# Kernel tuning notes

Hardware: AMD Instinct MI355X
Metric: run time of the kernel (lower is better)

Reference implementation:

```python
import jax, jax.numpy as jnp
import numpy as np

SQRT5 = 2.2360679774997896


def setup_inputs() -> dict:
    key = jax.random.key(0)
    k1, k2, k3 = jax.random.split(key, 3)
    n, m, d = 1024, 1024, 8
    X1 = jax.random.normal(k1, (n, d), dtype=jnp.float32)
    X2 = jax.random.normal(k2, (m, d), dtype=jnp.float32)
    c = jnp.asarray(1.0, dtype=jnp.float32)  # overall_scaling (scalar param)
    # character_length: positive lengthscales per feature
    l = 0.5 + jax.random.uniform(k3, (d,), dtype=jnp.float32)
    return {"X1": X1, "X2": X2, "c": c, "l": l}


def reference(X1, X2, c, l):
    # X1: [n, d], X2: [m, d] -> out [n, d, m, d]
    d = l.shape[0]
    inv_l2 = 1.0 / (l * l)                       # [d]
    DX1X2 = X1[:, None, :] - X2[None, :, :]      # [n, m, d]
    # scaled pairwise distance r[i,j] = || (X1_i - X2_j) / l ||
    r = jnp.sqrt(jnp.sum((DX1X2 / l) ** 2, axis=-1))   # [n, m]
    fr = (5.0 / 3.0) * jnp.exp(-SQRT5 * r)             # [n, m]
    # M[a,b] = (1/l^2) * eye(d) with column-wise broadcast (matches torch):
    M = inv_l2 * jnp.eye(d, dtype=l.dtype)             # [d, d], diag = 1/l^2
    A = fr * (1.0 + SQRT5 * r)                         # [n, m]
    D = DX1X2 * inv_l2                                 # [n, m, d]
    # k[i,a,j,b] = A[i,j]*M[a,b] - 5*fr[i,j]*D[i,j,a]*D[i,j,b]
    k = jnp.einsum('ij,ab->iajb', A, M) - 5.0 * jnp.einsum('ij,ija,ijb->iajb', fr, D, D)
    return (c * c) * k
```

## Files before the change

### kernel.cpp

```cpp
#include <hip/hip_runtime.h>

#define SQRT5F 2.2360679774997896f


__global__ __launch_bounds__(256) void deriv2_matern52_kernel(
    const float* __restrict__ X1,
    const float* __restrict__ X2,
    const float* __restrict__ c_ptr,
    const float* __restrict__ l_ptr,
    float* __restrict__ out,
    int m )
{
    const int t = threadIdx.x;
    const int jblocks = m >> 7;
    const int i  = blockIdx.x / jblocks;
    const int jb = blockIdx.x - i * jblocks;
    const int j  = (jb << 7) + (t >> 1);
    const int h  = t & 1;
    const int b0 = h << 2;

    const float c  = c_ptr[0];
    const float c2 = c * c;

    float inv_l2[8];
#pragma unroll
    for (int k = 0; k < 8; ++k) {
        const float lv = l_ptr[k];
        inv_l2[k] = 1.0f / (lv * lv);
    }

    const float4 x1a = ((const float4*)(X1 + (size_t)i * 8))[0];
    const float4 x1b = ((const float4*)(X1 + (size_t)i * 8))[1];
    const float4 x2a = ((const float4*)(X2 + (size_t)j * 8))[0];
    const float4 x2b = ((const float4*)(X2 + (size_t)j * 8))[1];

    const float dx[8] = { x1a.x - x2a.x, x1a.y - x2a.y, x1a.z - x2a.z, x1a.w - x2a.w,
                          x1b.x - x2b.x, x1b.y - x2b.y, x1b.z - x2b.z, x1b.w - x2b.w };

    float D[8];
    float r2 = 0.0f;
#pragma unroll
    for (int k = 0; k < 8; ++k) {
        D[k] = dx[k] * inv_l2[k];
        r2 += dx[k] * D[k];
    }

    const float r  = sqrtf(r2);
    const float fr = (5.0f / 3.0f) * expf(-SQRT5F * r);
    const float A  = fr * (1.0f + SQRT5F * r);

    const float Ac = A * c2;
    const float cf = -5.0f * fr * c2;

    const float Db[4] = { D[b0 + 0], D[b0 + 1], D[b0 + 2], D[b0 + 3] };

    float* op = out + (size_t)i * (size_t)(8 * m * 8) + (size_t)j * 8 + b0;
    const size_t astride = (size_t)m * 8;

#pragma unroll
    for (int a = 0; a < 8; ++a) {
        const float Dca = cf * D[a];
        float v[4];
#pragma unroll
        for (int k = 0; k < 4; ++k) v[k] = Dca * Db[k];
        const int da = a - b0;
        if (da >= 0 && da < 4) v[da] += Ac * inv_l2[a];

        *(float4*)(op + (size_t)a * astride) = make_float4(v[0], v[1], v[2], v[3]);
    }
}

extern "C" void kernel_launch(void* const* d_in, const int* in_sizes, int n_in,
                              void* d_out, int out_size, void* d_ws, size_t ws_size,
                              hipStream_t stream) {
    const float* X1 = (const float*)d_in[0];
    const float* X2 = (const float*)d_in[1];
    const float* c  = (const float*)d_in[2];
    const float* l  = (const float*)d_in[3];
    float* out = (float*)d_out;

    const int d = in_sizes[3];
    const int n = in_sizes[0] / d;
    const int m = in_sizes[1] / d;

    const int jblocks = m >> 7;
    dim3 grid(n * jblocks);
    dim3 block(256);
    deriv2_matern52_kernel<<<grid, block, 0, stream>>>(X1, X2, c, l, out, m);
}
```

Measured before the change: 257.5 us.

## Assign one output row per wavefront and loop over X2 in a persistent block

Each block now handles one X1 row with 512 threads, and each of its 8 wavefronts owns one output 'a' plane. Every lane loops over j in strides of 32 and writes one float4 per iteration, so a wavefront's stores form one contiguous 1KB run instead of eight strided stores per thread. The cost is that the distance and exp math is recomputed 8 times, once per wavefront, and the grid shrinks to n blocks, each running a sequential loop. Branchless selector masks replace the per-thread diagonal branch.

```diff
diff --git a/kernel.cpp b/kernel.cpp
--- a/kernel.cpp
+++ b/kernel.cpp
@@ -3,7 +3,7 @@
 #define SQRT5F 2.2360679774997896f
 
 
-__global__ __launch_bounds__(256) void deriv2_matern52_kernel(
+__global__ __launch_bounds__(512) void deriv2_matern52_kernel(
     const float* __restrict__ X1,
     const float* __restrict__ X2,
     const float* __restrict__ c_ptr,
@@ -11,13 +11,14 @@
     float* __restrict__ out,
     int m )
 {
-    const int t = threadIdx.x;
-    const int jblocks = m >> 7;
-    const int i  = blockIdx.x / jblocks;
-    const int jb = blockIdx.x - i * jblocks;
-    const int j  = (jb << 7) + (t >> 1);
-    const int h  = t & 1;
-    const int b0 = h << 2;
+    const int t    = threadIdx.x;
+    const int w    = t >> 6;
+    const int lane = t & 63;
+    const int p    = lane >> 1;
+    const int h    = lane & 1;
+    const int b0   = h << 2;
+
+    const int i = blockIdx.x;
 
     const float c  = c_ptr[0];
     const float c2 = c * c;
@@ -29,44 +30,67 @@
         inv_l2[k] = 1.0f / (lv * lv);
     }
 
+    float asel[8];
+#pragma unroll
+    for (int a = 0; a < 8; ++a) asel[a] = (a == w) ? 1.0f : 0.0f;
+
+    float il_w = 0.0f;
+#pragma unroll
+    for (int a = 0; a < 8; ++a) il_w = fmaf(asel[a], inv_l2[a], il_w);
+
+    float dk[4];
+#pragma unroll
+    for (int k = 0; k < 4; ++k)
+        dk[k] = (((w & 3) == k) && ((w >> 2) == h)) ? 1.0f : 0.0f;
+
     const float4 x1a = ((const float4*)(X1 + (size_t)i * 8))[0];
     const float4 x1b = ((const float4*)(X1 + (size_t)i * 8))[1];
-    const float4 x2a = ((const float4*)(X2 + (size_t)j * 8))[0];
-    const float4 x2b = ((const float4*)(X2 + (size_t)j * 8))[1];
+    const float x1v[8] = { x1a.x, x1a.y, x1a.z, x1a.w,
+                           x1b.x, x1b.y, x1b.z, x1b.w };
 
-    const float dx[8] = { x1a.x - x2a.x, x1a.y - x2a.y, x1a.z - x2a.z, x1a.w - x2a.w,
-                          x1b.x - x2b.x, x1b.y - x2b.y, x1b.z - x2b.z, x1b.w - x2b.w };
+    float* op = out + (size_t)i * (size_t)(8 * m * 8)
+                    + (size_t)w * (size_t)(m * 8)
+                    + (size_t)p * 8 + b0;
+    const float* xp = X2 + (size_t)p * 8;
 
-    float D[8];
-    float r2 = 0.0f;
+    for (int s = 0; s < m; s += 32) {
+        const float4 x2a = ((const float4*)xp)[0];
+        const float4 x2b = ((const float4*)xp)[1];
+        const float x2v[8] = { x2a.x, x2a.y, x2a.z, x2a.w,
+                               x2b.x, x2b.y, x2b.z, x2b.w };
+
+        float D[8];
+        float r2 = 0.0f;
 #pragma unroll
-    for (int k = 0; k < 8; ++k) {
-        D[k] = dx[k] * inv_l2[k];
-        r2 += dx[k] * D[k];
-    }
+        for (int k = 0; k < 8; ++k) {
+            const float dx = x1v[k] - x2v[k];
+            D[k] = dx * inv_l2[k];
+            r2 += dx * D[k];
+        }
 
-    const float r  = sqrtf(r2);
-    const float fr = (5.0f / 3.0f) * expf(-SQRT5F * r);
-    const float A  = fr * (1.0f + SQRT5F * r);
+        const float r  = sqrtf(r2);
+        const float fr = (5.0f / 3.0f) * expf(-SQRT5F * r);
+        const float A  = fr * (1.0f + SQRT5F * r);
 
-    const float Ac = A * c2;
-    const float cf = -5.0f * fr * c2;
+        const float Acil = A * c2 * il_w;
+        const float cf   = -5.0f * fr * c2;
 
-    const float Db[4] = { D[b0 + 0], D[b0 + 1], D[b0 + 2], D[b0 + 3] };
+        float Dw = 0.0f;
+#pragma unroll
+        for (int a = 0; a < 8; ++a) Dw = fmaf(asel[a], D[a], Dw);
+        const float Dca = cf * Dw;
 
-    float* op = out + (size_t)i * (size_t)(8 * m * 8) + (size_t)j * 8 + b0;
-    const size_t astride = (size_t)m * 8;
+        const float Db[4] = { D[b0 + 0], D[b0 + 1], D[b0 + 2], D[b0 + 3] };
 
-#pragma unroll
-    for (int a = 0; a < 8; ++a) {
-        const float Dca = cf * D[a];
         float v[4];
 #pragma unroll
-        for (int k = 0; k < 4; ++k) v[k] = Dca * Db[k];
-        const int da = a - b0;
-        if (da >= 0 && da < 4) v[da] += Ac * inv_l2[a];
+        for (int k = 0; k < 4; ++k)
+            v[k] = fmaf(dk[k], Acil, Dca * Db[k]);
 
-        *(float4*)(op + (size_t)a * astride) = make_float4(v[0], v[1], v[2], v[3]);
+        *(float4*)op = make_float4(v[0], v[1], v[2], v[3]);
+
+        op += 32 * 8;
+        xp += 32 * 8;
     }
 }
 
@@ -83,8 +107,7 @@
     const int n = in_sizes[0] / d;
     const int m = in_sizes[1] / d;
 
-    const int jblocks = m >> 7;
-    dim3 grid(n * jblocks);
-    dim3 block(256);
+    dim3 grid(n);
+    dim3 block(512);
     deriv2_matern52_kernel<<<grid, block, 0, stream>>>(X1, X2, c, l, out, m);
 }
```

After: 274.4 us. 6.5% more time.
